# Kernel optimization log

Hardware: AMD Instinct MI355X
Metric: run time of the kernel (lower is better)

Reference implementation:

```python
import jax, jax.numpy as jnp
import numpy as np

HIDDEN = 256

def setup_inputs() -> dict:
    key = jax.random.key(0)
    k1, k2, k3, k4, k5 = jax.random.split(key, 5)
    B, T, I, H = 1024, 336, 64, HIDDEN
    s = 1.0 / np.sqrt(H)  # PyTorch LSTM init scale
    return {
        "x": jax.random.normal(k1, (B, T, I), dtype=jnp.float32),
        "W_ih": jax.random.uniform(k2, (4 * H, I), dtype=jnp.float32, minval=-s, maxval=s),
        "W_hh": jax.random.uniform(k3, (4 * H, H), dtype=jnp.float32, minval=-s, maxval=s),
        "b_ih": jax.random.uniform(k4, (4 * H,), dtype=jnp.float32, minval=-s, maxval=s),
        "b_hh": jax.random.uniform(k5, (4 * H,), dtype=jnp.float32, minval=-s, maxval=s),
    }

def reference(x, W_ih, W_hh, b_ih, b_hh):
    # Single-layer unidirectional LSTM (batch_first), PyTorch gate order i,f,g,o.
    B, T, I = x.shape
    H = W_hh.shape[1]
    # Precompute input contribution for all timesteps: [T, B, 4H]
    x_gates = jnp.einsum('bti,gi->tbg', x, W_ih) + (b_ih + b_hh)

    def step(carry, xg_t):
        h, c = carry
        gates = xg_t + h @ W_hh.T          # [B, 4H]
        i, f, g, o = jnp.split(gates, 4, axis=-1)
        c_new = jax.nn.sigmoid(f) * c + jax.nn.sigmoid(i) * jnp.tanh(g)
        h_new = jax.nn.sigmoid(o) * jnp.tanh(c_new)
        return (h_new, c_new), None

    h0 = jnp.zeros((B, H), dtype=x.dtype)
    c0 = jnp.zeros((B, H), dtype=x.dtype)
    (hT, cT), _ = jax.lax.scan(step, (h0, c0), x_gates)
    # hn, cn shaped [num_layers*D, B, H] = [1, B, H]
    return hT[None], cT[None]
```

## Files before the change

### kernel.cpp

```cpp
#include <hip/hip_runtime.h>
#include <cstdint>


#define NGROUP  32
#define BATCH_G 32
#define T_STEPS 336
#define I_DIM   64
#define H_DIM   256
#define VSTRIDE 336
#define PAIRS   128
#define OUT_HALF 262144

typedef __attribute__((ext_vector_type(8))) __bf16 bf16x8;
typedef __attribute__((ext_vector_type(8))) unsigned short ushort8_t;
typedef __attribute__((ext_vector_type(4))) float f32x4;
typedef __attribute__((ext_vector_type(4))) unsigned uint32x4;
typedef __attribute__((ext_vector_type(2))) unsigned uint32x2;

__device__ inline unsigned short f2bf(float f) {
  unsigned u = __builtin_bit_cast(unsigned, f);
  return (unsigned short)((u + 0x7fffu + ((u >> 16) & 1u)) >> 16);
}
__device__ inline float sigf(float x) { return 1.f / (1.f + __expf(-x)); }
__device__ inline float tanhfast(float x) { return 1.f - 2.f / (1.f + __expf(2.f * x)); }

__device__ inline void ld4_tagged(const uint32x2* p, uint32x4& a, uint32x4& b,
                                  uint32x4& c, uint32x4& d) {
  asm volatile(
      "global_load_dwordx4 %0, %4, off sc0 sc1\n\t"
      "global_load_dwordx4 %1, %5, off sc0 sc1\n\t"
      "global_load_dwordx4 %2, %6, off sc0 sc1\n\t"
      "global_load_dwordx4 %3, %7, off sc0 sc1\n\t"
      "s_waitcnt vmcnt(0)"
      : "=&v"(a), "=&v"(b), "=&v"(c), "=&v"(d)
      : "v"(p), "v"(p + 2), "v"(p + 4), "v"(p + 6)
      : "memory");
}
__device__ inline void st_pair(uint32x2* p, uint32x2 v) {
  asm volatile("global_store_dwordx2 %0, %1, off sc0 sc1" :: "v"(p), "v"(v) : "memory");
}

__global__ __launch_bounds__(512, 2) void lstm_persistent(
    const float* __restrict__ x, const float* __restrict__ W_ih,
    const float* __restrict__ W_hh, const float* __restrict__ b_ih,
    const float* __restrict__ b_hh, float* __restrict__ out,
    uint32x2* __restrict__ hbuf)
{
  __shared__ __align__(16) unsigned short v_lds[2][BATCH_G * VSTRIDE];

  const int tid  = threadIdx.x;
  const int gid  = blockIdx.x & 31;
  const int mid  = blockIdx.x >> 5;
  const int wv   = tid >> 6;
  const int l    = tid & 63;
  const int l15  = l & 15, quad = l >> 4;
  const int rg   = wv >> 1;
  const int bh   = wv & 1;

  bf16x8 afrag[2][10];
#pragma unroll
  for (int rt = 0; rt < 2; ++rt) {
    int grow = (l15 & 3) * H_DIM + mid * 32 + rg * 8 + rt * 4 + (l15 >> 2);
    const float* wih_row = W_ih + (long)grow * I_DIM;
    const float* whh_row = W_hh + (long)grow * H_DIM;
#pragma unroll
    for (int kt = 0; kt < 10; ++kt) {
      int kbase = kt * 32 + quad * 8;
      ushort8_t a;
#pragma unroll
      for (int e = 0; e < 8; ++e) {
        int k = kbase + e;
        float v = (k < I_DIM) ? wih_row[k] : whh_row[k - I_DIM];
        a[e] = f2bf(v);
      }
      afrag[rt][kt] = __builtin_bit_cast(bf16x8, a);
    }
  }

  f32x4 bias[2];
#pragma unroll
  for (int rt = 0; rt < 2; ++rt) {
#pragma unroll
    for (int g = 0; g < 4; ++g) {
      int grow = g * H_DIM + mid * 32 + rg * 8 + rt * 4 + quad;
      bias[rt][g] = b_ih[grow] + b_hh[grow];
    }
  }

  const int batch = bh * 16 + l15;
  float c_reg[2] = {0.f, 0.f};
  float h_keep[2];

  const int b_stage = tid >> 4;
  const int x_i4    = (tid & 15) * 4;
  const long xrow_base = ((long)(gid * 32 + b_stage)) * T_STEPS * I_DIM;

  const int p_ld  = tid >> 2;
  const int b0_ld = (tid & 3) * 8;
  const uint32x2* ld_base = hbuf + ((long)gid * PAIRS + p_ld) * BATCH_G + b0_ld;

  uint32x2* st_base = hbuf + ((long)gid * PAIRS + mid * 16 + rg * 4 + (quad >> 1)) * BATCH_G + batch;
  const long buf_stride = (long)NGROUP * PAIRS * BATCH_G;
  const bool own_wave = (wv == mid);

  for (int t = 1; t <= T_STEPS; ++t) {
    unsigned short* vbuf = v_lds[t & 1];

    const float4 xv = *(const float4*)(x + xrow_base + (long)(t - 1) * I_DIM + x_i4);
    {
      ushort4 xb;
      xb.x = f2bf(xv.x); xb.y = f2bf(xv.y); xb.z = f2bf(xv.z); xb.w = f2bf(xv.w);
      *(ushort4*)&vbuf[b_stage * VSTRIDE + x_i4] = xb;
    }

    unsigned short* hdst = vbuf + b0_ld * VSTRIDE + I_DIM + 2 * p_ld;
    if (t > 1) {
      if (!own_wave) {
        const unsigned tag = (unsigned)(t - 1);
        const uint32x2* hsrc = ld_base + ((t - 1) & 1) * buf_stride;
        uint32x4 A, Bv, C, D;
        int it = 0;
        for (;;) {
          ld4_tagged(hsrc, A, Bv, C, D);
          bool ok = (A[0] == tag) & (A[2] == tag) & (Bv[0] == tag) & (Bv[2] == tag) &
                    (C[0] == tag) & (C[2] == tag) & (D[0] == tag) & (D[2] == tag);
          if (ok) break;
          if (++it > (1 << 17)) break;
          __builtin_amdgcn_s_sleep(1);
        }
        *(unsigned*)(hdst + 0 * VSTRIDE) = A[1];
        *(unsigned*)(hdst + 1 * VSTRIDE) = A[3];
        *(unsigned*)(hdst + 2 * VSTRIDE) = Bv[1];
        *(unsigned*)(hdst + 3 * VSTRIDE) = Bv[3];
        *(unsigned*)(hdst + 4 * VSTRIDE) = C[1];
        *(unsigned*)(hdst + 5 * VSTRIDE) = C[3];
        *(unsigned*)(hdst + 6 * VSTRIDE) = D[1];
        *(unsigned*)(hdst + 7 * VSTRIDE) = D[3];
      }
    } else {
#pragma unroll
      for (int j = 0; j < 8; ++j) *(unsigned*)(hdst + j * VSTRIDE) = 0u;
    }
    __syncthreads();

    f32x4 acc0 = bias[0], acc1 = bias[1];
    const unsigned short* vb = vbuf + (unsigned)batch * VSTRIDE + quad * 8;
#pragma unroll
    for (int kt = 0; kt < 10; ++kt) {
      bf16x8 bv = __builtin_bit_cast(bf16x8, *(const uint32x4*)(vb + kt * 32));
      acc0 = __builtin_amdgcn_mfma_f32_16x16x32_bf16(afrag[0][kt], bv, acc0, 0, 0, 0);
      acc1 = __builtin_amdgcn_mfma_f32_16x16x32_bf16(afrag[1][kt], bv, acc1, 0, 0, 0);
    }

    unsigned short* next_own = v_lds[(t + 1) & 1] + batch * VSTRIDE + I_DIM + mid * 32;
#pragma unroll
    for (int rt = 0; rt < 2; ++rt) {
      const f32x4 acc = rt ? acc1 : acc0;
      float c = sigf(acc[1]) * c_reg[rt] + sigf(acc[0]) * tanhfast(acc[2]);
      float h = sigf(acc[3]) * tanhfast(c);
      c_reg[rt] = c; h_keep[rt] = h;
      unsigned short hb16 = f2bf(h);
      next_own[rg * 8 + rt * 4 + quad] = hb16;
      unsigned hb = (unsigned)hb16;
      unsigned partner = (unsigned)__shfl_xor((int)hb, 16, 64);
      if (!(quad & 1)) {
        uint32x2 pv;
        pv[0] = (unsigned)t;
        pv[1] = hb | (partner << 16);
        st_pair(st_base + rt * 2 * BATCH_G + (t & 1) * buf_stride, pv);
      }
    }
  }

#pragma unroll
  for (int rt = 0; rt < 2; ++rt) {
    int gcol = mid * 32 + rg * 8 + rt * 4 + quad;
    long o = (long)(gid * BATCH_G + batch) * H_DIM + gcol;
    out[o]            = h_keep[rt];
    out[OUT_HALF + o] = c_reg[rt];
  }
}

extern "C" void kernel_launch(void* const* d_in, const int* in_sizes, int n_in,
                              void* d_out, int out_size, void* d_ws, size_t ws_size,
                              hipStream_t stream) {
  const float* x    = (const float*)d_in[0];
  const float* W_ih = (const float*)d_in[1];
  const float* W_hh = (const float*)d_in[2];
  const float* b_ih = (const float*)d_in[3];
  const float* b_hh = (const float*)d_in[4];
  float* out = (float*)d_out;

  uint32x2* hbuf = (uint32x2*)d_ws;

  hipMemsetAsync(d_ws, 0, 2u * NGROUP * PAIRS * BATCH_G * 8u, stream);
  lstm_persistent<<<dim3(256), dim3(512), 0, stream>>>(x, W_ih, W_hh, b_ih, b_hh, out, hbuf);
}
```

Measured before the change: 981.9 us.

## Remap blocks to XCDs so group exchanges use XCD-local cache coherence

Blocks read their hardware XCD id, register it in a global counter table, and then assign group and member ids so that the 8 blocks of each LSTM batch group tend to sit on the same XCD. A startup probe checks whether the group's members can see each other's stores with only sc0 (L2-level) coherence. If they can, the per-step h exchange drops the sc1 system-coherent bits and polls at L2 scope, avoiding round trips through the slower device-wide coherence point. The change also prefetches the next timestep's x row one step ahead and pads the LDS row stride to reduce bank conflicts. These gains come at the cost of a startup all-block barrier and probe, and correctness relies on the runtime probe choosing the coherence mode properly.

```diff
diff --git a/kernel.cpp b/kernel.cpp
--- a/kernel.cpp
+++ b/kernel.cpp
@@ -7,9 +7,10 @@
 #define T_STEPS 336
 #define I_DIM   64
 #define H_DIM   256
-#define VSTRIDE 336
+#define VSTRIDE 344
 #define PAIRS   128
 #define OUT_HALF 262144
+#define MAGIC   0x7F7F7F7Fu
 
 typedef __attribute__((ext_vector_type(8))) __bf16 bf16x8;
 typedef __attribute__((ext_vector_type(8))) unsigned short ushort8_t;
@@ -24,38 +25,130 @@
 __device__ inline float sigf(float x) { return 1.f / (1.f + __expf(-x)); }
 __device__ inline float tanhfast(float x) { return 1.f - 2.f / (1.f + __expf(2.f * x)); }
 
+template<bool DEV>
 __device__ inline void ld4_tagged(const uint32x2* p, uint32x4& a, uint32x4& b,
                                   uint32x4& c, uint32x4& d) {
-  asm volatile(
-      "global_load_dwordx4 %0, %4, off sc0 sc1\n\t"
-      "global_load_dwordx4 %1, %5, off sc0 sc1\n\t"
-      "global_load_dwordx4 %2, %6, off sc0 sc1\n\t"
-      "global_load_dwordx4 %3, %7, off sc0 sc1\n\t"
-      "s_waitcnt vmcnt(0)"
-      : "=&v"(a), "=&v"(b), "=&v"(c), "=&v"(d)
-      : "v"(p), "v"(p + 2), "v"(p + 4), "v"(p + 6)
-      : "memory");
-}
+  if constexpr (DEV) {
+    asm volatile(
+        "global_load_dwordx4 %0, %4, off sc0 sc1\n\t"
+        "global_load_dwordx4 %1, %5, off sc0 sc1\n\t"
+        "global_load_dwordx4 %2, %6, off sc0 sc1\n\t"
+        "global_load_dwordx4 %3, %7, off sc0 sc1\n\t"
+        "s_waitcnt vmcnt(0)"
+        : "=&v"(a), "=&v"(b), "=&v"(c), "=&v"(d)
+        : "v"(p), "v"(p + 2), "v"(p + 4), "v"(p + 6)
+        : "memory");
+  } else {
+    asm volatile(
+        "global_load_dwordx4 %0, %4, off sc0\n\t"
+        "global_load_dwordx4 %1, %5, off sc0\n\t"
+        "global_load_dwordx4 %2, %6, off sc0\n\t"
+        "global_load_dwordx4 %3, %7, off sc0\n\t"
+        "s_waitcnt vmcnt(0)"
+        : "=&v"(a), "=&v"(b), "=&v"(c), "=&v"(d)
+        : "v"(p), "v"(p + 2), "v"(p + 4), "v"(p + 6)
+        : "memory");
+  }
+}
+template<bool DEV>
 __device__ inline void st_pair(uint32x2* p, uint32x2 v) {
-  asm volatile("global_store_dwordx2 %0, %1, off sc0 sc1" :: "v"(p), "v"(v) : "memory");
+  if constexpr (DEV) {
+    asm volatile("global_store_dwordx2 %0, %1, off sc0 sc1" :: "v"(p), "v"(v) : "memory");
+  } else {
+    asm volatile("global_store_dwordx2 %0, %1, off sc0" :: "v"(p), "v"(v) : "memory");
+  }
+}
+
+template<bool DEV>
+__device__ inline void stage_h(const uint32x2* hsrc, unsigned tag, unsigned short* hdst) {
+  uint32x4 A, Bv, C, D;
+  int it = 0;
+  for (;;) {
+    ld4_tagged<DEV>(hsrc, A, Bv, C, D);
+    bool ok = (A[0] == tag) & (A[2] == tag) & (Bv[0] == tag) & (Bv[2] == tag) &
+              (C[0] == tag) & (C[2] == tag) & (D[0] == tag) & (D[2] == tag);
+    if (ok) break;
+    if (++it > (1 << 17)) break;
+    __builtin_amdgcn_s_sleep(1);
+  }
+  *(unsigned*)(hdst + 0 * VSTRIDE) = A[1];
+  *(unsigned*)(hdst + 1 * VSTRIDE) = A[3];
+  *(unsigned*)(hdst + 2 * VSTRIDE) = Bv[1];
+  *(unsigned*)(hdst + 3 * VSTRIDE) = Bv[3];
+  *(unsigned*)(hdst + 4 * VSTRIDE) = C[1];
+  *(unsigned*)(hdst + 5 * VSTRIDE) = C[3];
+  *(unsigned*)(hdst + 6 * VSTRIDE) = D[1];
+  *(unsigned*)(hdst + 7 * VSTRIDE) = D[3];
+}
+
+__device__ inline bool probe_poll(const uint32x2* p) {
+  uint32x4 A, Bv, C, D;
+  for (int it = 0; it < 512; ++it) {
+    ld4_tagged<false>(p, A, Bv, C, D);
+    bool ok = (A[0] == MAGIC) & (A[2] == MAGIC) & (Bv[0] == MAGIC) & (Bv[2] == MAGIC) &
+              (C[0] == MAGIC) & (C[2] == MAGIC) & (D[0] == MAGIC) & (D[2] == MAGIC);
+    if (ok) return true;
+    __builtin_amdgcn_s_sleep(1);
+  }
+  return false;
 }
 
 __global__ __launch_bounds__(512, 2) void lstm_persistent(
     const float* __restrict__ x, const float* __restrict__ W_ih,
     const float* __restrict__ W_hh, const float* __restrict__ b_ih,
     const float* __restrict__ b_hh, float* __restrict__ out,
-    uint32x2* __restrict__ hbuf)
+    uint32x2* __restrict__ hbuf, unsigned* __restrict__ xtab)
 {
   __shared__ __align__(16) unsigned short v_lds[2][BATCH_G * VSTRIDE];
+  __shared__ int s_same, s_ok;
+  __shared__ unsigned s_cnt[8], s_xcd, s_rank;
 
   const int tid  = threadIdx.x;
-  const int gid  = blockIdx.x & 31;
-  const int mid  = blockIdx.x >> 5;
   const int wv   = tid >> 6;
   const int l    = tid & 63;
   const int l15  = l & 15, quad = l >> 4;
   const int rg   = wv >> 1;
   const int bh   = wv & 1;
+
+  unsigned* cnt   = xtab;
+  unsigned* vslot = xtab + 8;
+
+  if (tid == 0) {
+    unsigned xcd = (unsigned)__builtin_amdgcn_s_getreg((31u << 11) | 20u) & 7u;
+    s_xcd  = xcd;
+    s_rank = __hip_atomic_fetch_add(&cnt[xcd], 1u, __ATOMIC_ACQ_REL,
+                                    __HIP_MEMORY_SCOPE_AGENT);
+    for (int itr = 0; itr < (1 << 26); ++itr) {
+      unsigned tot = 0;
+      for (int xx = 0; xx < 8; ++xx)
+        tot += __hip_atomic_load(&cnt[xx], __ATOMIC_ACQUIRE, __HIP_MEMORY_SCOPE_AGENT);
+      if (tot >= 256u) break;
+      __builtin_amdgcn_s_sleep(4);
+    }
+    for (int xx = 0; xx < 8; ++xx)
+      s_cnt[xx] = __hip_atomic_load(&cnt[xx], __ATOMIC_ACQUIRE, __HIP_MEMORY_SCOPE_AGENT);
+  }
+  __syncthreads();
+
+  int gid, mid;
+  {
+    const unsigned xcd = s_xcd, rank = s_rank;
+    unsigned prefFull = 0, prefLeft = 0, totalFull = 0;
+    for (unsigned xx = 0; xx < 8; ++xx) {
+      unsigned n = s_cnt[xx], f = n >> 3;
+      totalFull += f;
+      if (xx < xcd) { prefFull += f; prefLeft += n - (f << 3); }
+    }
+    const unsigned fullx = (s_cnt[xcd] >> 3) << 3;
+    if (rank < fullx) {
+      gid = (int)(prefFull + (rank >> 3));
+      mid = (int)(rank & 7u);
+    } else {
+      unsigned li = prefLeft + (rank - fullx);
+      gid = (int)(totalFull + (li >> 3));
+      mid = (int)(li & 7u);
+    }
+  }
 
   bf16x8 afrag[2][10];
 #pragma unroll
@@ -93,7 +186,7 @@
 
   const int b_stage = tid >> 4;
   const int x_i4    = (tid & 15) * 4;
-  const long xrow_base = ((long)(gid * 32 + b_stage)) * T_STEPS * I_DIM;
+  const float* xrow = x + ((long)(gid * 32 + b_stage)) * T_STEPS * I_DIM + x_i4;
 
   const int p_ld  = tid >> 2;
   const int b0_ld = (tid & 3) * 8;
@@ -103,39 +196,58 @@
   const long buf_stride = (long)NGROUP * PAIRS * BATCH_G;
   const bool own_wave = (wv == mid);
 
+  if (!(quad & 1)) {
+#pragma unroll
+    for (int rt = 0; rt < 2; ++rt) {
+      uint32x2 pv; pv[0] = MAGIC; pv[1] = MAGIC;
+      st_pair<false>(st_base + rt * 2 * BATCH_G, pv);
+    }
+  }
+  const bool okp = probe_poll(ld_base);
+  if (tid == 0) s_ok = 1;
+  __syncthreads();
+  if (!okp) s_ok = 0;
+  __syncthreads();
+  if (tid == 0) {
+    __hip_atomic_store(&vslot[gid * 8 + mid], (unsigned)(s_ok ? 2 : 1),
+                       __ATOMIC_RELEASE, __HIP_MEMORY_SCOPE_AGENT);
+    int verdict = 0;
+    for (int itr = 0; itr < (1 << 24); ++itr) {
+      bool all = true, good = true;
+#pragma unroll
+      for (int m = 0; m < 8; ++m) {
+        unsigned v = __hip_atomic_load(&vslot[gid * 8 + m], __ATOMIC_ACQUIRE,
+                                       __HIP_MEMORY_SCOPE_AGENT);
+        all &= (v != 0u);
+        good &= (v == 2u);
+      }
+      if (all) { verdict = good ? 1 : 0; break; }
+      __builtin_amdgcn_s_sleep(4);
+    }
+    s_same = verdict;
+  }
+  __syncthreads();
+  const bool same_xcd = (s_same != 0);
+
+  float4 xv = *(const float4*)xrow;
+
   for (int t = 1; t <= T_STEPS; ++t) {
     unsigned short* vbuf = v_lds[t & 1];
 
-    const float4 xv = *(const float4*)(x + xrow_base + (long)(t - 1) * I_DIM + x_i4);
     {
       ushort4 xb;
       xb.x = f2bf(xv.x); xb.y = f2bf(xv.y); xb.z = f2bf(xv.z); xb.w = f2bf(xv.w);
       *(ushort4*)&vbuf[b_stage * VSTRIDE + x_i4] = xb;
     }
+    if (t < T_STEPS) xv = *(const float4*)(xrow + (long)t * I_DIM);
 
     unsigned short* hdst = vbuf + b0_ld * VSTRIDE + I_DIM + 2 * p_ld;
     if (t > 1) {
       if (!own_wave) {
         const unsigned tag = (unsigned)(t - 1);
         const uint32x2* hsrc = ld_base + ((t - 1) & 1) * buf_stride;
-        uint32x4 A, Bv, C, D;
-        int it = 0;
-        for (;;) {
-          ld4_tagged(hsrc, A, Bv, C, D);
-          bool ok = (A[0] == tag) & (A[2] == tag) & (Bv[0] == tag) & (Bv[2] == tag) &
-                    (C[0] == tag) & (C[2] == tag) & (D[0] == tag) & (D[2] == tag);
-          if (ok) break;
-          if (++it > (1 << 17)) break;
-          __builtin_amdgcn_s_sleep(1);
-        }
-        *(unsigned*)(hdst + 0 * VSTRIDE) = A[1];
-        *(unsigned*)(hdst + 1 * VSTRIDE) = A[3];
-        *(unsigned*)(hdst + 2 * VSTRIDE) = Bv[1];
-        *(unsigned*)(hdst + 3 * VSTRIDE) = Bv[3];
-        *(unsigned*)(hdst + 4 * VSTRIDE) = C[1];
-        *(unsigned*)(hdst + 5 * VSTRIDE) = C[3];
-        *(unsigned*)(hdst + 6 * VSTRIDE) = D[1];
-        *(unsigned*)(hdst + 7 * VSTRIDE) = D[3];
+        if (same_xcd) stage_h<false>(hsrc, tag, hdst);
+        else          stage_h<true >(hsrc, tag, hdst);
       }
     } else {
 #pragma unroll
@@ -167,7 +279,9 @@
         uint32x2 pv;
         pv[0] = (unsigned)t;
         pv[1] = hb | (partner << 16);
-        st_pair(st_base + rt * 2 * BATCH_G + (t & 1) * buf_stride, pv);
+        uint32x2* dst = st_base + rt * 2 * BATCH_G + (t & 1) * buf_stride;
+        if (same_xcd) st_pair<false>(dst, pv);
+        else          st_pair<true >(dst, pv);
       }
     }
   }
@@ -192,7 +306,8 @@
   float* out = (float*)d_out;
 
   uint32x2* hbuf = (uint32x2*)d_ws;
-
-  hipMemsetAsync(d_ws, 0, 2u * NGROUP * PAIRS * BATCH_G * 8u, stream);
-  lstm_persistent<<<dim3(256), dim3(512), 0, stream>>>(x, W_ih, W_hh, b_ih, b_hh, out, hbuf);
-}
+  unsigned* xtab = (unsigned*)((char*)d_ws + 2u * NGROUP * PAIRS * BATCH_G * 8u);
+
+  hipMemsetAsync(d_ws, 0, 2u * NGROUP * PAIRS * BATCH_G * 8u + 2048u, stream);
+  lstm_persistent<<<dim3(256), dim3(512), 0, stream>>>(x, W_ih, W_hh, b_ih, b_hh, out, hbuf, xtab);
+}
```

After: 1.745 ms. 1.78x slower.

## Repartition LSTM work into 4-block groups and prefetch x one step ahead

Applied to the files above, without the earlier changes.

Each block now covers 64 hidden units for 16 batch rows instead of 32 units for 32 rows. Each recurrent exchange therefore involves 4 cooperating blocks instead of 8, and each thread polls and stages half as much tagged h data per step. The next timestep's x slice is loaded one iteration early to hide global load latency. The gate/state update is wrapped in s_setprio so the critical path of the recurrence gets scheduling priority. In exchange, the MFMA B operand now carries only 16 batch rows, and the per-block weight fragment set covers a different slice of the gate rows.

```diff
diff --git a/kernel.cpp b/kernel.cpp
--- a/kernel.cpp
+++ b/kernel.cpp
@@ -2,8 +2,8 @@
 #include <cstdint>
 
 
-#define NGROUP  32
-#define BATCH_G 32
+#define NGROUP  64
+#define BATCH_G 16
 #define T_STEPS 336
 #define I_DIM   64
 #define H_DIM   256
@@ -24,20 +24,33 @@
 __device__ inline float sigf(float x) { return 1.f / (1.f + __expf(-x)); }
 __device__ inline float tanhfast(float x) { return 1.f - 2.f / (1.f + __expf(2.f * x)); }
 
-__device__ inline void ld4_tagged(const uint32x2* p, uint32x4& a, uint32x4& b,
-                                  uint32x4& c, uint32x4& d) {
+__device__ inline void ld2_tagged(const uint32x2* p, uint32x4& a, uint32x4& b) {
   asm volatile(
-      "global_load_dwordx4 %0, %4, off sc0 sc1\n\t"
-      "global_load_dwordx4 %1, %5, off sc0 sc1\n\t"
-      "global_load_dwordx4 %2, %6, off sc0 sc1\n\t"
-      "global_load_dwordx4 %3, %7, off sc0 sc1\n\t"
+      "global_load_dwordx4 %0, %2, off sc0 sc1\n\t"
+      "global_load_dwordx4 %1, %3, off sc0 sc1\n\t"
       "s_waitcnt vmcnt(0)"
-      : "=&v"(a), "=&v"(b), "=&v"(c), "=&v"(d)
-      : "v"(p), "v"(p + 2), "v"(p + 4), "v"(p + 6)
+      : "=&v"(a), "=&v"(b)
+      : "v"(p), "v"(p + 2)
       : "memory");
 }
 __device__ inline void st_pair(uint32x2* p, uint32x2 v) {
   asm volatile("global_store_dwordx2 %0, %1, off sc0 sc1" :: "v"(p), "v"(v) : "memory");
+}
+
+__device__ inline void stage_h(const uint32x2* hsrc, unsigned tag, unsigned short* hdst) {
+  uint32x4 A, Bv;
+  int it = 0;
+  for (;;) {
+    ld2_tagged(hsrc, A, Bv);
+    bool ok = (A[0] == tag) & (A[2] == tag) & (Bv[0] == tag) & (Bv[2] == tag);
+    if (ok) break;
+    if (++it > (1 << 17)) break;
+    __builtin_amdgcn_s_sleep(1);
+  }
+  *(unsigned*)(hdst + 0 * VSTRIDE) = A[1];
+  *(unsigned*)(hdst + 1 * VSTRIDE) = A[3];
+  *(unsigned*)(hdst + 2 * VSTRIDE) = Bv[1];
+  *(unsigned*)(hdst + 3 * VSTRIDE) = Bv[3];
 }
 
 __global__ __launch_bounds__(512, 2) void lstm_persistent(
@@ -49,18 +62,17 @@
   __shared__ __align__(16) unsigned short v_lds[2][BATCH_G * VSTRIDE];
 
   const int tid  = threadIdx.x;
-  const int gid  = blockIdx.x & 31;
-  const int mid  = blockIdx.x >> 5;
+  const int gid  = blockIdx.x & 63;
+  const int mid  = blockIdx.x >> 6;
   const int wv   = tid >> 6;
   const int l    = tid & 63;
   const int l15  = l & 15, quad = l >> 4;
-  const int rg   = wv >> 1;
-  const int bh   = wv & 1;
+  const int rg   = wv;
 
   bf16x8 afrag[2][10];
 #pragma unroll
   for (int rt = 0; rt < 2; ++rt) {
-    int grow = (l15 & 3) * H_DIM + mid * 32 + rg * 8 + rt * 4 + (l15 >> 2);
+    int grow = (l15 & 3) * H_DIM + mid * 64 + rg * 8 + rt * 4 + (l15 >> 2);
     const float* wih_row = W_ih + (long)grow * I_DIM;
     const float* whh_row = W_hh + (long)grow * H_DIM;
 #pragma unroll
@@ -82,64 +94,49 @@
   for (int rt = 0; rt < 2; ++rt) {
 #pragma unroll
     for (int g = 0; g < 4; ++g) {
-      int grow = g * H_DIM + mid * 32 + rg * 8 + rt * 4 + quad;
+      int grow = g * H_DIM + mid * 64 + rg * 8 + rt * 4 + quad;
       bias[rt][g] = b_ih[grow] + b_hh[grow];
     }
   }
 
-  const int batch = bh * 16 + l15;
+  const int batch = l15;
   float c_reg[2] = {0.f, 0.f};
   float h_keep[2];
 
-  const int b_stage = tid >> 4;
-  const int x_i4    = (tid & 15) * 4;
-  const long xrow_base = ((long)(gid * 32 + b_stage)) * T_STEPS * I_DIM;
+  const int b_stage = tid >> 5;
+  const int x_i2    = (tid & 31) * 2;
+  const float* xrow = x + ((long)(gid * BATCH_G + b_stage)) * T_STEPS * I_DIM + x_i2;
 
   const int p_ld  = tid >> 2;
-  const int b0_ld = (tid & 3) * 8;
+  const int b0_ld = (tid & 3) * 4;
   const uint32x2* ld_base = hbuf + ((long)gid * PAIRS + p_ld) * BATCH_G + b0_ld;
 
-  uint32x2* st_base = hbuf + ((long)gid * PAIRS + mid * 16 + rg * 4 + (quad >> 1)) * BATCH_G + batch;
+  uint32x2* st_base = hbuf + ((long)gid * PAIRS + mid * 32 + rg * 4 + (quad >> 1)) * BATCH_G + batch;
   const long buf_stride = (long)NGROUP * PAIRS * BATCH_G;
-  const bool own_wave = (wv == mid);
+  const bool own_wave = ((wv >> 1) == mid);
+
+  float2 xv = *(const float2*)xrow;
 
   for (int t = 1; t <= T_STEPS; ++t) {
     unsigned short* vbuf = v_lds[t & 1];
 
-    const float4 xv = *(const float4*)(x + xrow_base + (long)(t - 1) * I_DIM + x_i4);
     {
-      ushort4 xb;
-      xb.x = f2bf(xv.x); xb.y = f2bf(xv.y); xb.z = f2bf(xv.z); xb.w = f2bf(xv.w);
-      *(ushort4*)&vbuf[b_stage * VSTRIDE + x_i4] = xb;
+      ushort2 xb;
+      xb.x = f2bf(xv.x); xb.y = f2bf(xv.y);
+      *(ushort2*)&vbuf[b_stage * VSTRIDE + x_i2] = xb;
     }
+    if (t < T_STEPS) xv = *(const float2*)(xrow + (long)t * I_DIM);
 
     unsigned short* hdst = vbuf + b0_ld * VSTRIDE + I_DIM + 2 * p_ld;
     if (t > 1) {
       if (!own_wave) {
         const unsigned tag = (unsigned)(t - 1);
         const uint32x2* hsrc = ld_base + ((t - 1) & 1) * buf_stride;
-        uint32x4 A, Bv, C, D;
-        int it = 0;
-        for (;;) {
-          ld4_tagged(hsrc, A, Bv, C, D);
-          bool ok = (A[0] == tag) & (A[2] == tag) & (Bv[0] == tag) & (Bv[2] == tag) &
-                    (C[0] == tag) & (C[2] == tag) & (D[0] == tag) & (D[2] == tag);
-          if (ok) break;
-          if (++it > (1 << 17)) break;
-          __builtin_amdgcn_s_sleep(1);
-        }
-        *(unsigned*)(hdst + 0 * VSTRIDE) = A[1];
-        *(unsigned*)(hdst + 1 * VSTRIDE) = A[3];
-        *(unsigned*)(hdst + 2 * VSTRIDE) = Bv[1];
-        *(unsigned*)(hdst + 3 * VSTRIDE) = Bv[3];
-        *(unsigned*)(hdst + 4 * VSTRIDE) = C[1];
-        *(unsigned*)(hdst + 5 * VSTRIDE) = C[3];
-        *(unsigned*)(hdst + 6 * VSTRIDE) = D[1];
-        *(unsigned*)(hdst + 7 * VSTRIDE) = D[3];
+        stage_h(hsrc, tag, hdst);
       }
     } else {
 #pragma unroll
-      for (int j = 0; j < 8; ++j) *(unsigned*)(hdst + j * VSTRIDE) = 0u;
+      for (int j = 0; j < 4; ++j) *(unsigned*)(hdst + j * VSTRIDE) = 0u;
     }
     __syncthreads();
 
@@ -152,7 +149,8 @@
       acc1 = __builtin_amdgcn_mfma_f32_16x16x32_bf16(afrag[1][kt], bv, acc1, 0, 0, 0);
     }
 
-    unsigned short* next_own = v_lds[(t + 1) & 1] + batch * VSTRIDE + I_DIM + mid * 32;
+    __builtin_amdgcn_s_setprio(1);
+    unsigned short* next_own = v_lds[(t + 1) & 1] + batch * VSTRIDE + I_DIM + mid * 64;
 #pragma unroll
     for (int rt = 0; rt < 2; ++rt) {
       const f32x4 acc = rt ? acc1 : acc0;
@@ -170,11 +168,12 @@
         st_pair(st_base + rt * 2 * BATCH_G + (t & 1) * buf_stride, pv);
       }
     }
+    __builtin_amdgcn_s_setprio(0);
   }
 
 #pragma unroll
   for (int rt = 0; rt < 2; ++rt) {
-    int gcol = mid * 32 + rg * 8 + rt * 4 + quad;
+    int gcol = mid * 64 + rg * 8 + rt * 4 + quad;
     long o = (long)(gid * BATCH_G + batch) * H_DIM + gcol;
     out[o]            = h_keep[rt];
     out[OUT_HALF + o] = c_reg[rt];
```

Result: faster. 916.5 us (-6.7%).
